# Optimization experiments

Measured on AMD Instinct MI355X. Metric: run time of the kernel, lower is better.

Reference implementation:

```python
import jax, jax.numpy as jnp
import numpy as np

B, T, V, D, H, E, K = 512, 80, 80, 128, 256, 8, 2
G1, G2 = 512, 256
EPS = 1e-5


def setup_inputs() -> dict:
    key = jax.random.key(0)
    ks = jax.random.split(key, 16)
    s = 0.05
    x = jax.random.randint(ks[0], (B, T), 0, V)
    emb = jax.random.normal(ks[1], (E, V, D), jnp.float32) * s
    Wih0 = jax.random.normal(ks[2], (E, 4 * H, D), jnp.float32) * s
    Whh0 = jax.random.normal(ks[3], (E, 4 * H, H), jnp.float32) * s
    bih0 = jnp.zeros((E, 4 * H), jnp.float32)
    bhh0 = jnp.zeros((E, 4 * H), jnp.float32)
    Wih1 = jax.random.normal(ks[4], (E, 4 * H, H), jnp.float32) * s
    Whh1 = jax.random.normal(ks[5], (E, 4 * H, H), jnp.float32) * s
    bih1 = jnp.zeros((E, 4 * H), jnp.float32)
    bhh1 = jnp.zeros((E, 4 * H), jnp.float32)
    fcw = jax.random.normal(ks[6], (E, V, H), jnp.float32) * s
    fcb = jnp.zeros((E, V), jnp.float32)
    gw1 = jax.random.normal(ks[7], (G1, D), jnp.float32) * s
    gb1 = jnp.zeros((G1,), jnp.float32)
    bn1_g = jnp.ones((G1,), jnp.float32)
    bn1_b = jnp.zeros((G1,), jnp.float32)
    bn1_m = jnp.zeros((G1,), jnp.float32)
    bn1_v = jnp.ones((G1,), jnp.float32)
    gw2 = jax.random.normal(ks[8], (G2, G1), jnp.float32) * s
    gb2 = jnp.zeros((G2,), jnp.float32)
    bn2_g = jnp.ones((G2,), jnp.float32)
    bn2_b = jnp.zeros((G2,), jnp.float32)
    bn2_m = jnp.zeros((G2,), jnp.float32)
    bn2_v = jnp.ones((G2,), jnp.float32)
    gw3 = jax.random.normal(ks[9], (E, G2), jnp.float32) * s
    gb3 = jnp.zeros((E,), jnp.float32)
    return dict(x=x, emb=emb, Wih0=Wih0, Whh0=Whh0, bih0=bih0, bhh0=bhh0,
                Wih1=Wih1, Whh1=Whh1, bih1=bih1, bhh1=bhh1, fcw=fcw, fcb=fcb,
                gw1=gw1, gb1=gb1, bn1_g=bn1_g, bn1_b=bn1_b, bn1_m=bn1_m, bn1_v=bn1_v,
                gw2=gw2, gb2=gb2, bn2_g=bn2_g, bn2_b=bn2_b, bn2_m=bn2_m, bn2_v=bn2_v,
                gw3=gw3, gb3=gb3)


def _lstm_layer(Wih, Whh, bih, bhh, xs):
    # xs: [B, T, Din] -> (hidden seq [B, T, H], final hidden [B, H]); torch gate order i,f,g,o
    h0 = jnp.zeros((xs.shape[0], Whh.shape[1]), xs.dtype)

    def step(carry, xt):
        h, c = carry
        z = xt @ Wih.T + bih + h @ Whh.T + bhh
        i, f, g, o = jnp.split(z, 4, axis=-1)
        c = jax.nn.sigmoid(f) * c + jax.nn.sigmoid(i) * jnp.tanh(g)
        h = jax.nn.sigmoid(o) * jnp.tanh(c)
        return (h, c), h

    (h, _), hs = jax.lax.scan(step, (h0, h0), jnp.swapaxes(xs, 0, 1))
    return jnp.swapaxes(hs, 0, 1), h


def _expert(emb_e, Wih0, Whh0, bih0, bhh0, Wih1, Whh1, bih1, bhh1, fcw, fcb, x):
    e = emb_e[x]                                   # [B, T, D]
    hs1, _ = _lstm_layer(Wih0, Whh0, bih0, bhh0, e)
    _, h2 = _lstm_layer(Wih1, Whh1, bih1, bhh1, hs1)
    return h2 @ fcw.T + fcb                        # [B, V] (fc on last timestep)


def _bn_eval(x, g, b, m, v):
    return (x - m) * jax.lax.rsqrt(v + EPS) * g + b


def _forward(x, emb, Wih0, Whh0, bih0, bhh0, Wih1, Whh1, bih1, bhh1, fcw, fcb,
             gw1, gb1, bn1_g, bn1_b, bn1_m, bn1_v,
             gw2, gb2, bn2_g, bn2_b, bn2_m, bn2_v, gw3, gb3):
    # gating features: expert 0 embedding, mean over time  [B, D]
    feat = emb[0][x].mean(axis=1)
    h = jax.nn.relu(_bn_eval(feat @ gw1.T + gb1, bn1_g, bn1_b, bn1_m, bn1_v))
    h = jax.nn.relu(_bn_eval(h @ gw2.T + gb2, bn2_g, bn2_b, bn2_m, bn2_v))
    logits = h @ gw3.T + gb3                       # [B, E]  (eval: no noise)
    scores = jax.nn.softmax(logits, axis=-1)
    tv, ti = jax.lax.top_k(scores, K)              # [B, K]
    w = tv / tv.sum(axis=-1, keepdims=True)
    # per-expert combine weight (top-k indices are distinct, at most one slot per expert)
    we = (w[..., None] * jax.nn.one_hot(ti, E, dtype=w.dtype)).sum(axis=1)  # [B, E]
    eouts = jax.vmap(_expert, in_axes=(0,) * 11 + (None,))(
        emb, Wih0, Whh0, bih0, bhh0, Wih1, Whh1, bih1, bhh1, fcw, fcb, x)   # [E, B, V]
    return jnp.einsum('ebc,be->bc', eouts, we)


def reference(x, emb, Wih0, Whh0, bih0, bhh0, Wih1, Whh1, bih1, bhh1, fcw, fcb,
              gw1, gb1, bn1_g, bn1_b, bn1_m, bn1_v,
              gw2, gb2, bn2_g, bn2_b, bn2_m, bn2_v, gw3, gb3):
    return _forward(x, emb, Wih0, Whh0, bih0, bhh0, Wih1, Whh1, bih1, bhh1, fcw, fcb,
                    gw1, gb1, bn1_g, bn1_b, bn1_m, bn1_v,
                    gw2, gb2, bn2_g, bn2_b, bn2_m, bn2_v, gw3, gb3)
```

## Files before the change

### kernel.cpp

```cpp
#include <hip/hip_runtime.h>
#include <hip/hip_bf16.h>
#include <math.h>

#define BB 512
#define TT 80
#define VV 80
#define DD 128
#define HH 256
#define FH 1024
#define EE 8
#define GG1 512
#define GG2 256
#define MT 16
#define NT 72
#define SLOTS (NT*MT)
#define CCK 16

typedef __attribute__((ext_vector_type(8))) short bf16x8;
typedef __attribute__((ext_vector_type(4))) float f32x4;
typedef __attribute__((ext_vector_type(4))) unsigned int u32x4;

__device__ __forceinline__ float bf2f(unsigned short u) {
    unsigned int v = ((unsigned int)u) << 16;
    return __builtin_bit_cast(float, v);
}
__device__ __forceinline__ unsigned short f2bf(float f) {
    __hip_bfloat16 h = __float2bfloat16(f);
    return __builtin_bit_cast(unsigned short, h);
}
__device__ __forceinline__ float sigm(float x) { return 1.f / (1.f + __expf(-x)); }
__device__ __forceinline__ float tanh_f(float x) {
    float ax = fabsf(x);
    float r = 1.f - 2.f / (__expf(2.f * ax) + 1.f);
    return x < 0.f ? -r : r;
}

__global__ void prep_kernel(const float* __restrict__ Whh0, const float* __restrict__ Wih1,
                            const float* __restrict__ Whh1,
                            const float* __restrict__ bih1, const float* __restrict__ bhh1,
                            unsigned short* __restrict__ WR0, unsigned short* __restrict__ WR1,
                            unsigned short* __restrict__ WG, float* __restrict__ bsum1)
{
    const int NB = 262144;
    const int ntot = 3 * NB + EE * FH;
    for (int idx = blockIdx.x * blockDim.x + threadIdx.x; idx < ntot;
         idx += gridDim.x * blockDim.x) {
        if (idx < 3 * NB) {
            int arr = idx / NB;
            int p = idx - arr * NB;
            int gc, kk, e;
            const float* src;
            if (arr < 2) {
                int l = p & 63, nf = (p >> 6) & 7, kb = (p >> 9) & 7, w = (p >> 12) & 7;
                e = (p >> 15) & 7;
                int g = nf >> 1, hc = nf & 1;
                gc = g * 256 + w * 32 + hc * 16 + (l & 15);
                kk = kb * 32 + ((l >> 4) * 8);
                src = (arr == 0) ? Whh0 : Whh1;
            } else {
                int l = p & 63, kb = (p >> 6) & 7, gf = (p >> 9) & 63; e = (p >> 15) & 7;
                gc = gf * 16 + (l & 15);
                kk = kb * 32 + ((l >> 4) * 8);
                src = Wih1;
            }
            const float* sp = src + ((size_t)e * FH + gc) * HH + kk;
            float4 f0 = *(const float4*)sp;
            float4 f1 = *(const float4*)(sp + 4);
            unsigned short out[8];
            out[0] = f2bf(f0.x); out[1] = f2bf(f0.y); out[2] = f2bf(f0.z); out[3] = f2bf(f0.w);
            out[4] = f2bf(f1.x); out[5] = f2bf(f1.y); out[6] = f2bf(f1.z); out[7] = f2bf(f1.w);
            unsigned short* dst = (arr == 0 ? WR0 : arr == 1 ? WR1 : WG) + (size_t)p * 8;
            *(uint4*)dst = *(uint4*)out;
        } else {
            int p = idx - 3 * NB;
            bsum1[p] = bih1[p] + bhh1[p];
        }
    }
}

__global__ __launch_bounds__(256)
void embw_kernel(const float* __restrict__ emb, const float* __restrict__ Wih0,
                 const float* __restrict__ bih0, const float* __restrict__ bhh0,
                 unsigned short* __restrict__ embT)
{
    const int e = blockIdx.x, g = blockIdx.y;
    const int tid = threadIdx.x;
    const int gc = g * 256 + tid;
    __shared__ float er[DD * VV];
    for (int i = tid; i < VV * DD; i += 256) {
        int tok = i >> 7, d = i & 127;
        er[d * VV + tok] = emb[((size_t)e * VV + tok) * DD + d];
    }
    __syncthreads();
    float acc[VV];
    #pragma unroll
    for (int v = 0; v < VV; v++) acc[v] = 0.f;
    const float* wr = Wih0 + ((size_t)e * FH + gc) * DD;
    for (int d = 0; d < DD; d++) {
        float wv = wr[d];
        #pragma unroll
        for (int v4 = 0; v4 < VV; v4 += 4) {
            float4 ev = *(const float4*)&er[d * VV + v4];
            acc[v4] += ev.x * wv; acc[v4 + 1] += ev.y * wv;
            acc[v4 + 2] += ev.z * wv; acc[v4 + 3] += ev.w * wv;
        }
    }
    float bias = bih0[e * FH + gc] + bhh0[e * FH + gc];
    #pragma unroll 4
    for (int v = 0; v < VV; v++)
        embT[(((size_t)e * VV + v) * 256 + tid) * 4 + g] = f2bf(acc[v] + bias);
}

__global__ __launch_bounds__(128)
void gating_kernel(const int* __restrict__ x, const float* __restrict__ emb,
                   const float* __restrict__ gw1, const float* __restrict__ gb1,
                   const float* __restrict__ g1g, const float* __restrict__ g1b,
                   const float* __restrict__ g1m, const float* __restrict__ g1v,
                   const float* __restrict__ gw2, const float* __restrict__ gb2,
                   const float* __restrict__ g2g, const float* __restrict__ g2b,
                   const float* __restrict__ g2m, const float* __restrict__ g2v,
                   const float* __restrict__ gw3, const float* __restrict__ gb3,
                   int* __restrict__ route_i, float* __restrict__ route_w)
{
    int b = blockIdx.x, tid = threadIdx.x;
    __shared__ int tk[TT];
    __shared__ float feat[DD];
    __shared__ float h1[GG1];
    __shared__ float h2[GG2];
    __shared__ float lg[EE];
    if (tid < TT) tk[tid] = x[b * TT + tid];
    __syncthreads();
    if (tid < DD) {
        float s = 0.f;
        for (int t = 0; t < TT; t++) s += emb[(size_t)tk[t] * DD + tid];
        feat[tid] = s * (1.f / TT);
    }
    __syncthreads();
    for (int j = tid; j < GG1; j += 128) {
        float s = gb1[j];
        const float* wr = gw1 + (size_t)j * DD;
        for (int d = 0; d < DD; d++) s += feat[d] * wr[d];
        float y = (s - g1m[j]) / sqrtf(g1v[j] + 1e-5f) * g1g[j] + g1b[j];
        h1[j] = y > 0.f ? y : 0.f;
    }
    __syncthreads();
    for (int j = tid; j < GG2; j += 128) {
        float s = gb2[j];
        const float* wr = gw2 + (size_t)j * GG1;
        for (int d = 0; d < GG1; d++) s += h1[d] * wr[d];
        float y = (s - g2m[j]) / sqrtf(g2v[j] + 1e-5f) * g2g[j] + g2b[j];
        h2[j] = y > 0.f ? y : 0.f;
    }
    __syncthreads();
    if (tid < EE) {
        float s = gb3[tid];
        const float* wr = gw3 + (size_t)tid * GG2;
        for (int d = 0; d < GG2; d++) s += h2[d] * wr[d];
        lg[tid] = s;
    }
    __syncthreads();
    if (tid == 0) {
        int i0 = 0;
        for (int i = 1; i < EE; i++) if (lg[i] > lg[i0]) i0 = i;
        int i1 = (i0 == 0) ? 1 : 0;
        for (int i = 0; i < EE; i++) if (i != i0 && lg[i] > lg[i1]) i1 = i;
        float e1 = expf(lg[i1] - lg[i0]);
        float inv = 1.f / (1.f + e1);
        route_i[b * 2] = i0; route_i[b * 2 + 1] = i1;
        route_w[b * 2] = inv; route_w[b * 2 + 1] = e1 * inv;
    }
}

__global__ __launch_bounds__(1024)
void route_kernel(const int* __restrict__ route_i, const float* __restrict__ route_w,
                  int* __restrict__ slot_b, int* __restrict__ slot_k,
                  float* __restrict__ slot_w, int* __restrict__ slot_e)
{
    __shared__ int wcnt[16][EE];
    __shared__ int cnt[EE];
    __shared__ int off[EE + 1];
    int tid = threadIdx.x;
    int lane = tid & 63, wv = tid >> 6;
    int e = route_i[tid];
    unsigned long long below = (1ull << lane) - 1ull;
    int rankw = 0;
    #pragma unroll
    for (int q = 0; q < EE; q++) {
        unsigned long long m = __ballot(e == q);
        if (q == e) rankw = __popcll(m & below);
        if (lane == 0) wcnt[wv][q] = __popcll(m);
    }
    __syncthreads();
    if (tid < EE) {
        int c = 0;
        for (int w2 = 0; w2 < 16; w2++) c += wcnt[w2][tid];
        cnt[tid] = c;
    }
    __syncthreads();
    if (tid == 0) {
        off[0] = 0;
        for (int q = 0; q < EE; q++) off[q + 1] = off[q] + ((cnt[q] + MT - 1) / MT) * MT;
    }
    __syncthreads();
    for (int s = tid; s < SLOTS; s += 1024) {
        int e2 = 0;
        if (s < off[EE]) { for (int q = 0; q < EE; q++) if (s >= off[q]) e2 = q; }
        slot_b[s] = -1; slot_k[s] = 0; slot_w[s] = 0.f; slot_e[s] = e2;
    }
    __syncthreads();
    int rank = rankw;
    for (int w2 = 0; w2 < wv; w2++) rank += wcnt[w2][e];
    int s = off[e] + rank;
    slot_b[s] = tid >> 1; slot_k[s] = tid & 1; slot_w[s] = route_w[tid];
}

template<int LAYER>
__device__ __forceinline__ void lstm_body(
    int t0, int tcount,
    const unsigned short* __restrict__ WR,
    const unsigned short* __restrict__ embT,
    const unsigned short* __restrict__ zin,
    const int* __restrict__ x,
    const int* __restrict__ slot_b, const int* __restrict__ slot_e,
    unsigned short* __restrict__ h0seq, float* __restrict__ h1f,
    float* __restrict__ cst, unsigned short* __restrict__ hsv,
    unsigned short (*wlds)[8][8][512], unsigned short (*hbuf)[4096], int* toks)
{
    const int tile = blockIdx.x;
    if (slot_b[tile * MT] < 0) return;
    const int tid = threadIdx.x;
    const int lane = tid & 63;
    const int w = tid >> 6;
    const int e = slot_e[tile * MT];
    const int l15 = lane & 15;
    const int q = lane >> 4;
    const int col0 = w * 32 + l15;
    const int col1 = col0 + 16;
    const int sc0 = (((col0 >> 5) * 64 + 16 * ((col0 >> 3) & 3)) << 3) + (col0 & 7);
    const int sc1 = (((col1 >> 5) * 64 + 16 * ((col1 >> 3) & 3)) << 3) + (col1 & 7);

    const unsigned short* WBg = WR + ((size_t)(e * 8 + w) * 64) * 512 + (size_t)lane * 8;

    u32x4 wres[32];
    #pragma unroll
    for (int i = 0; i < 32; i++) wres[i] = *(const u32x4*)(WBg + (size_t)i * 512);
    #pragma unroll
    for (int i = 0; i < 32; i++) asm volatile("" : "+v"(wres[i]));

    #pragma unroll
    for (int i = 0; i < 16; i++)
        *(uint4*)&wlds[i >> 3][w][i & 7][lane * 8] = *(const uint4*)(WBg + (size_t)(32 + i) * 512);

    if (LAYER == 0) {
        for (int i = tid; i < tcount * 16; i += 512)
            toks[i] = x[max(slot_b[tile * MT + (i & 15)], 0) * TT + t0 + (i >> 4)];
    }

    if (t0 == 0) {
        *(f32x4*)&hbuf[0][tid * 8] = (f32x4){0.f, 0.f, 0.f, 0.f};
    } else {
        *(bf16x8*)&hbuf[0][tid * 8] = *(const bf16x8*)(hsv + (size_t)tile * 4096 + tid * 8);
    }
    float c[8];
    if (t0 == 0) {
        #pragma unroll
        for (int i = 0; i < 8; i++) c[i] = 0.f;
    } else {
        f32x4 v0 = *(const f32x4*)&cst[((size_t)(tile * 512 + tid)) * 8];
        f32x4 v1 = *(const f32x4*)&cst[((size_t)(tile * 512 + tid)) * 8 + 4];
        c[0]=v0[0]; c[1]=v0[1]; c[2]=v0[2]; c[3]=v0[3];
        c[4]=v1[0]; c[5]=v1[1]; c[6]=v1[2]; c[7]=v1[3];
    }

    __syncthreads();

    ushort4 za[4], zb[4];
    if (LAYER == 0) {
        #pragma unroll
        for (int reg = 0; reg < 4; reg++) {
            int tok = toks[q * 4 + reg];
            const unsigned short* zp = embT + ((size_t)(e * VV + tok)) * 1024;
            za[reg] = *(const ushort4*)(zp + col0 * 4);
            zb[reg] = *(const ushort4*)(zp + col1 * 4);
        }
    } else {
        const unsigned short* zp = zin + ((size_t)(tile * tcount)) * 16384;
        #pragma unroll
        for (int g = 0; g < 4; g++) {
            int gfa = g * 16 + w * 2;
            za[g] = *(const ushort4*)(zp + (gfa * 64 + lane) * 4);
            zb[g] = *(const ushort4*)(zp + ((gfa + 1) * 64 + lane) * 4);
        }
    }

    int cur = 0;
    for (int t = 0; t < tcount; t++) {
        const int nxt = cur ^ 1;

        ushort4 zan[4], zbn[4];
        {
            int tn = (t + 1 < tcount) ? t + 1 : t;
            if (LAYER == 0) {
                #pragma unroll
                for (int reg = 0; reg < 4; reg++) {
                    int tok = toks[tn * 16 + q * 4 + reg];
                    const unsigned short* zp = embT + ((size_t)(e * VV + tok)) * 1024;
                    zan[reg] = *(const ushort4*)(zp + col0 * 4);
                    zbn[reg] = *(const ushort4*)(zp + col1 * 4);
                }
            } else {
                const unsigned short* zp = zin + ((size_t)(tile * tcount + tn)) * 16384;
                #pragma unroll
                for (int g = 0; g < 4; g++) {
                    int gfa = g * 16 + w * 2;
                    zan[g] = *(const ushort4*)(zp + (gfa * 64 + lane) * 4);
                    zbn[g] = *(const ushort4*)(zp + ((gfa + 1) * 64 + lane) * 4);
                }
            }
        }

        u32x4 ws[8];
        #pragma unroll
        for (int nf = 0; nf < 8; nf++) ws[nf] = *(const u32x4*)(WBg + (size_t)(48 + nf) * 512);

        f32x4 acc[8];
        if (LAYER == 0) {
            #pragma unroll
            for (int reg = 0; reg < 4; reg++) {
                acc[0][reg] = bf2f(za[reg].x); acc[2][reg] = bf2f(za[reg].y);
                acc[4][reg] = bf2f(za[reg].z); acc[6][reg] = bf2f(za[reg].w);
                acc[1][reg] = bf2f(zb[reg].x); acc[3][reg] = bf2f(zb[reg].y);
                acc[5][reg] = bf2f(zb[reg].z); acc[7][reg] = bf2f(zb[reg].w);
            }
        } else {
            #pragma unroll
            for (int g = 0; g < 4; g++) {
                acc[g * 2][0] = bf2f(za[g].x); acc[g * 2][1] = bf2f(za[g].y);
                acc[g * 2][2] = bf2f(za[g].z); acc[g * 2][3] = bf2f(za[g].w);
                acc[g * 2 + 1][0] = bf2f(zb[g].x); acc[g * 2 + 1][1] = bf2f(zb[g].y);
                acc[g * 2 + 1][2] = bf2f(zb[g].z); acc[g * 2 + 1][3] = bf2f(zb[g].w);
            }
        }

        #pragma unroll
        for (int kb = 0; kb < 4; kb++) {
            bf16x8 a = *(const bf16x8*)&hbuf[cur][(kb * 64 + lane) * 8];
            #pragma unroll
            for (int nf = 0; nf < 8; nf++)
                acc[nf] = __builtin_amdgcn_mfma_f32_16x16x32_bf16(
                    a, __builtin_bit_cast(bf16x8, wres[kb * 8 + nf]), acc[nf], 0, 0, 0);
        }

        #pragma unroll
        for (int kbi = 0; kbi < 2; kbi++) {
            bf16x8 a = *(const bf16x8*)&hbuf[cur][((4 + kbi) * 64 + lane) * 8];
            #pragma unroll
            for (int nf = 0; nf < 8; nf++) {
                bf16x8 wl = *(const bf16x8*)&wlds[kbi][w][nf][lane * 8];
                acc[nf] = __builtin_amdgcn_mfma_f32_16x16x32_bf16(a, wl, acc[nf], 0, 0, 0);
            }
        }

        {
            bf16x8 a = *(const bf16x8*)&hbuf[cur][(6 * 64 + lane) * 8];
            #pragma unroll
            for (int nf = 0; nf < 8; nf++)
                acc[nf] = __builtin_amdgcn_mfma_f32_16x16x32_bf16(
                    a, __builtin_bit_cast(bf16x8, ws[nf]), acc[nf], 0, 0, 0);
        }
        #pragma unroll
        for (int nf = 0; nf < 8; nf++) ws[nf] = *(const u32x4*)(WBg + (size_t)(56 + nf) * 512);
        {
            bf16x8 a = *(const bf16x8*)&hbuf[cur][(7 * 64 + lane) * 8];
            #pragma unroll
            for (int nf = 0; nf < 8; nf++)
                acc[nf] = __builtin_amdgcn_mfma_f32_16x16x32_bf16(
                    a, __builtin_bit_cast(bf16x8, ws[nf]), acc[nf], 0, 0, 0);
        }

        #pragma unroll
        for (int reg = 0; reg < 4; reg++) {
            int r = q * 4 + reg;
            {
                float iv = acc[0][reg], fv = acc[2][reg], gv = acc[4][reg], ov = acc[6][reg];
                float cn = sigm(fv) * c[reg * 2] + sigm(iv) * tanh_f(gv);
                float hn = sigm(ov) * tanh_f(cn);
                c[reg * 2] = cn;
                hbuf[nxt][sc0 + r * 8] = f2bf(hn);
                if (LAYER == 1 && t0 + t == TT - 1)
                    h1f[((size_t)(tile * MT + r)) * HH + col0] = hn;
            }
            {
                float iv = acc[1][reg], fv = acc[3][reg], gv = acc[5][reg], ov = acc[7][reg];
                float cn = sigm(fv) * c[reg * 2 + 1] + sigm(iv) * tanh_f(gv);
                float hn = sigm(ov) * tanh_f(cn);
                c[reg * 2 + 1] = cn;
                hbuf[nxt][sc1 + r * 8] = f2bf(hn);
                if (LAYER == 1 && t0 + t == TT - 1)
                    h1f[((size_t)(tile * MT + r)) * HH + col1] = hn;
            }
        }
        __syncthreads();
        cur = nxt;
        #pragma unroll
        for (int i = 0; i < 4; i++) { za[i] = zan[i]; zb[i] = zbn[i]; }
        if (LAYER == 0) {
            *(uint4*)(h0seq + ((size_t)(tile * tcount + t)) * 4096 + tid * 8) =
                *(const uint4*)&hbuf[cur][tid * 8];
        }
    }

    f32x4 v0, v1;
    v0[0]=c[0]; v0[1]=c[1]; v0[2]=c[2]; v0[3]=c[3];
    v1[0]=c[4]; v1[1]=c[5]; v1[2]=c[6]; v1[3]=c[7];
    *(f32x4*)&cst[((size_t)(tile * 512 + tid)) * 8] = v0;
    *(f32x4*)&cst[((size_t)(tile * 512 + tid)) * 8 + 4] = v1;
    *(uint4*)(hsv + (size_t)tile * 4096 + tid * 8) = *(const uint4*)&hbuf[cur][tid * 8];
}

__device__ __forceinline__ void gemm_body(
    int tcount,
    const unsigned short* __restrict__ h0seq,
    const unsigned short* __restrict__ WG,
    const float* __restrict__ bsum1,
    const int* __restrict__ slot_b, const int* __restrict__ slot_e,
    unsigned short* __restrict__ zin1,
    unsigned short* Abuf)
{
    const int tile = blockIdx.x;
    if (slot_b[tile * MT] < 0) return;
    const int tid = threadIdx.x, lane = tid & 63, w = tid >> 6;
    const int e = slot_e[tile * MT];
    const int l15 = lane & 15;
    for (int tch = 0; tch < tcount / 8; tch++) {
        const unsigned short* Asrc = h0seq + ((size_t)(tile * tcount + tch * 8)) * 4096;
        #pragma unroll
        for (int i = 0; i < 8; i++) {
            int o = (i * 512 + tid) * 8;
            *(bf16x8*)&Abuf[o] = *(const bf16x8*)&Asrc[o];
        }
        __syncthreads();
        #pragma unroll
        for (int gh = 0; gh < 2; gh++) {
            const unsigned short* Bp = WG + ((size_t)(e * 64 + w * 8 + gh * 4)) * 4096 + (size_t)lane * 8;
            f32x4 acc[8][4];
            #pragma unroll
            for (int mf = 0; mf < 8; mf++)
                #pragma unroll
                for (int nfi = 0; nfi < 4; nfi++) acc[mf][nfi] = (f32x4){0.f, 0.f, 0.f, 0.f};
            #pragma unroll
            for (int kb = 0; kb < 8; kb++) {
                bf16x8 b0 = *(const bf16x8*)(Bp + 0 * 4096 + kb * 512);
                bf16x8 b1 = *(const bf16x8*)(Bp + 1 * 4096 + kb * 512);
                bf16x8 b2 = *(const bf16x8*)(Bp + 2 * 4096 + kb * 512);
                bf16x8 b3 = *(const bf16x8*)(Bp + 3 * 4096 + kb * 512);
                #pragma unroll
                for (int mf = 0; mf < 8; mf++) {
                    bf16x8 a = *(const bf16x8*)&Abuf[(mf * 8 + kb) * 512 + lane * 8];
                    acc[mf][0] = __builtin_amdgcn_mfma_f32_16x16x32_bf16(a, b0, acc[mf][0], 0, 0, 0);
                    acc[mf][1] = __builtin_amdgcn_mfma_f32_16x16x32_bf16(a, b1, acc[mf][1], 0, 0, 0);
                    acc[mf][2] = __builtin_amdgcn_mfma_f32_16x16x32_bf16(a, b2, acc[mf][2], 0, 0, 0);
                    acc[mf][3] = __builtin_amdgcn_mfma_f32_16x16x32_bf16(a, b3, acc[mf][3], 0, 0, 0);
                }
            }
            #pragma unroll
            for (int mf = 0; mf < 8; mf++) {
                unsigned short* ob = zin1 + ((size_t)(tile * tcount + tch * 8 + mf)) * 16384;
                #pragma unroll
                for (int nfi = 0; nfi < 4; nfi++) {
                    int gf = w * 8 + gh * 4 + nfi;
                    float bs = bsum1[e * FH + gf * 16 + l15];
                    ushort4 v;
                    v.x = f2bf(acc[mf][nfi][0] + bs);
                    v.y = f2bf(acc[mf][nfi][1] + bs);
                    v.z = f2bf(acc[mf][nfi][2] + bs);
                    v.w = f2bf(acc[mf][nfi][3] + bs);
                    *(ushort4*)(ob + (size_t)(gf * 64 + lane) * 4) = v;
                }
            }
        }
        __syncthreads();
    }
}

__global__ __launch_bounds__(512, 1)
void lstm_fused(int t00, int t01, int tg, int tcount,
                const unsigned short* __restrict__ WR0, const unsigned short* __restrict__ WR1,
                const unsigned short* __restrict__ WG, const float* __restrict__ bsum1,
                const unsigned short* __restrict__ embT,
                unsigned short* __restrict__ h0_w, const unsigned short* __restrict__ h0_r,
                unsigned short* __restrict__ zin_w, const unsigned short* __restrict__ zin_r,
                const int* __restrict__ x,
                const int* __restrict__ slot_b, const int* __restrict__ slot_e,
                float* __restrict__ h1f,
                float* __restrict__ cst0, float* __restrict__ cst1,
                unsigned short* __restrict__ hsv0, unsigned short* __restrict__ hsv1)
{
    __shared__ unsigned short wlds[2][8][8][512];
    __shared__ unsigned short hbuf[2][4096];
    __shared__ int toks[CCK * 16];
    if (blockIdx.y == 0) {
        if (t00 < 0) return;
        lstm_body<0>(t00, tcount, WR0, embT, nullptr, x, slot_b, slot_e,
                     h0_w, h1f, cst0, hsv0, wlds, hbuf, toks);
    } else if (blockIdx.y == 1) {
        if (t01 < 0) return;
        lstm_body<1>(t01, tcount, WR1, embT, zin_r, x, slot_b, slot_e,
                     nullptr, h1f, cst1, hsv1, wlds, hbuf, toks);
    } else {
        if (tg < 0) return;
        gemm_body(tcount, h0_r, WG, bsum1, slot_b, slot_e, zin_w, &wlds[0][0][0][0]);
    }
}

__global__ __launch_bounds__(256)
void fc_kernel(const float* __restrict__ fcw, const float* __restrict__ fcb,
               const float* __restrict__ h1f,
               const int* __restrict__ slot_b, const int* __restrict__ slot_k,
               const float* __restrict__ slot_w, const int* __restrict__ slot_e,
               float* __restrict__ wout)
{
    int s = blockIdx.x;
    int b = slot_b[s];
    if (b < 0) return;
    int tid = threadIdx.x;
    __shared__ float hv[HH];
    if (tid < HH) hv[tid] = h1f[(size_t)s * HH + tid];
    __syncthreads();
    int e = slot_e[s], kk = slot_k[s];
    float w = slot_w[s];
    for (int v = tid; v < VV; v += 256) {
        float sacc = fcb[e * VV + v];
        const float* fr = fcw + ((size_t)e * VV + v) * HH;
        #pragma unroll 4
        for (int d = 0; d < HH; d++) sacc += hv[d] * fr[d];
        wout[((size_t)b * 2 + kk) * VV + v] = w * sacc;
    }
}

__global__ void combine_kernel(const float* __restrict__ wout, float* __restrict__ out)
{
    int i = blockIdx.x * blockDim.x + threadIdx.x;
    if (i < BB * VV) {
        int b = i / VV, v = i % VV;
        out[i] = wout[((size_t)b * 2) * VV + v] + wout[((size_t)b * 2 + 1) * VV + v];
    }
}

extern "C" void kernel_launch(void* const* d_in, const int* in_sizes, int n_in,
                              void* d_out, int out_size, void* d_ws, size_t ws_size,
                              hipStream_t stream)
{
    const int*   x    = (const int*)d_in[0];
    const float* emb  = (const float*)d_in[1];
    const float* Wih0 = (const float*)d_in[2];
    const float* Whh0 = (const float*)d_in[3];
    const float* bih0 = (const float*)d_in[4];
    const float* bhh0 = (const float*)d_in[5];
    const float* Wih1 = (const float*)d_in[6];
    const float* Whh1 = (const float*)d_in[7];
    const float* bih1 = (const float*)d_in[8];
    const float* bhh1 = (const float*)d_in[9];
    const float* fcw  = (const float*)d_in[10];
    const float* fcb  = (const float*)d_in[11];
    const float* gw1  = (const float*)d_in[12];
    const float* gb1  = (const float*)d_in[13];
    const float* b1g  = (const float*)d_in[14];
    const float* b1b  = (const float*)d_in[15];
    const float* b1m  = (const float*)d_in[16];
    const float* b1v  = (const float*)d_in[17];
    const float* gw2  = (const float*)d_in[18];
    const float* gb2  = (const float*)d_in[19];
    const float* b2g  = (const float*)d_in[20];
    const float* b2b  = (const float*)d_in[21];
    const float* b2m  = (const float*)d_in[22];
    const float* b2v  = (const float*)d_in[23];
    const float* gw3  = (const float*)d_in[24];
    const float* gb3  = (const float*)d_in[25];

    const size_t NWsh = 262144 * 8;

    char* base = (char*)d_ws;
    size_t o = 0;
    auto alloc = [&](size_t bytes) { char* p = base + o; o = (o + bytes + 255) & ~(size_t)255; return p; };

    unsigned short* WR0  = (unsigned short*)alloc(NWsh * 2);
    unsigned short* WR1  = (unsigned short*)alloc(NWsh * 2);
    unsigned short* WG   = (unsigned short*)alloc(NWsh * 2);
    unsigned short* embT = (unsigned short*)alloc((size_t)EE * VV * FH * 2);
    float* bsum1 = (float*)alloc((size_t)EE * FH * 4);
    float* h1f   = (float*)alloc((size_t)SLOTS * HH * 4);
    float* wout  = (float*)alloc((size_t)BB * 2 * VV * 4);
    float* cst0  = (float*)alloc((size_t)NT * 512 * 8 * 4);
    float* cst1  = (float*)alloc((size_t)NT * 512 * 8 * 4);
    unsigned short* hsv0 = (unsigned short*)alloc((size_t)NT * 4096 * 2);
    unsigned short* hsv1 = (unsigned short*)alloc((size_t)NT * 4096 * 2);
    float* route_w = (float*)alloc((size_t)BB * 2 * 4);
    float* slot_w  = (float*)alloc((size_t)SLOTS * 4);
    int* route_i = (int*)alloc((size_t)BB * 2 * 4);
    int* slot_b  = (int*)alloc((size_t)SLOTS * 4);
    int* slot_k  = (int*)alloc((size_t)SLOTS * 4);
    int* slot_e  = (int*)alloc((size_t)SLOTS * 4);
    unsigned short* h0seqA = (unsigned short*)alloc((size_t)NT * CCK * 4096 * 2);
    unsigned short* h0seqB = (unsigned short*)alloc((size_t)NT * CCK * 4096 * 2);
    unsigned short* zinA   = (unsigned short*)alloc((size_t)NT * CCK * 16384 * 2);
    unsigned short* zinB   = (unsigned short*)alloc((size_t)NT * CCK * 16384 * 2);

    prep_kernel<<<3104, 256, 0, stream>>>(Whh0, Wih1, Whh1, bih1, bhh1, WR0, WR1, WG, bsum1);
    embw_kernel<<<dim3(EE, 4), 256, 0, stream>>>(emb, Wih0, bih0, bhh0, embT);
    gating_kernel<<<BB, 128, 0, stream>>>(x, emb, gw1, gb1, b1g, b1b, b1m, b1v,
                                          gw2, gb2, b2g, b2b, b2m, b2v, gw3, gb3,
                                          route_i, route_w);
    route_kernel<<<1, 1024, 0, stream>>>(route_i, route_w, slot_b, slot_k, slot_w, slot_e);

    const int nch = TT / CCK;
    for (int ph = 0; ph <= nch + 1; ph++) {
        int t00 = (ph < nch) ? ph * CCK : -1;
        int tg  = (ph - 1 >= 0 && ph - 1 < nch) ? (ph - 1) * CCK : -1;
        int t01 = (ph - 2 >= 0 && ph - 2 < nch) ? (ph - 2) * CCK : -1;
        unsigned short* h0_w = (ph & 1) ? h0seqB : h0seqA;
        unsigned short* h0_r = ((ph - 1) & 1) ? h0seqB : h0seqA;
        unsigned short* zn_w = ((ph - 1) & 1) ? zinB : zinA;
        unsigned short* zn_r = ((ph - 2) & 1) ? zinB : zinA;
        lstm_fused<<<dim3(NT, 3), 512, 0, stream>>>(t00, t01, tg, CCK, WR0, WR1, WG, bsum1,
                                                    embT, h0_w, h0_r, zn_w, zn_r, x,
                                                    slot_b, slot_e, h1f,
                                                    cst0, cst1, hsv0, hsv1);
    }

    fc_kernel<<<SLOTS, 256, 0, stream>>>(fcw, fcb, h1f, slot_b, slot_k, slot_w, slot_e, wout);
    combine_kernel<<<(BB * VV + 255) / 256, 256, 0, stream>>>(wout, (float*)d_out);
}
```

Before: 775.4 us.

## Replace per-phase kernel launches with one persistent cooperative kernel using grid sync

```diff
diff --git a/kernel.cpp b/kernel.cpp
--- a/kernel.cpp
+++ b/kernel.cpp
@@ -1,6 +1,9 @@
 #include <hip/hip_runtime.h>
 #include <hip/hip_bf16.h>
+#include <hip/hip_cooperative_groups.h>
 #include <math.h>
+
+namespace cg = cooperative_groups;
 
 #define BB 512
 #define TT 80
@@ -15,6 +18,8 @@
 #define NT 72
 #define SLOTS (NT*MT)
 #define CCK 16
+#define NCH (TT/CCK)
+#define NPH (NCH+2)
 
 typedef __attribute__((ext_vector_type(8))) short bf16x8;
 typedef __attribute__((ext_vector_type(4))) float f32x4;
@@ -215,23 +220,16 @@
 }
 
 template<int LAYER>
-__device__ __forceinline__ void lstm_body(
-    int t0, int tcount,
-    const unsigned short* __restrict__ WR,
+__device__ __forceinline__ void lstm_chunk(
+    int t0, int tile, int e, int lane, int w,
+    const unsigned short* __restrict__ WBg,
     const unsigned short* __restrict__ embT,
     const unsigned short* __restrict__ zin,
-    const int* __restrict__ x,
-    const int* __restrict__ slot_b, const int* __restrict__ slot_e,
-    unsigned short* __restrict__ h0seq, float* __restrict__ h1f,
-    float* __restrict__ cst, unsigned short* __restrict__ hsv,
-    unsigned short (*wlds)[8][8][512], unsigned short (*hbuf)[4096], int* toks)
-{
-    const int tile = blockIdx.x;
-    if (slot_b[tile * MT] < 0) return;
-    const int tid = threadIdx.x;
-    const int lane = tid & 63;
-    const int w = tid >> 6;
-    const int e = slot_e[tile * MT];
+    unsigned short* __restrict__ h0_w, float* __restrict__ h1f,
+    u32x4 (&wres)[32],
+    unsigned short (*wlds)[8][8][512], unsigned short (*hbuf)[4096], int* toks,
+    float (&c)[8], int& cur)
+{
     const int l15 = lane & 15;
     const int q = lane >> 4;
     const int col0 = w * 32 + l15;
@@ -239,52 +237,17 @@
     const int sc0 = (((col0 >> 5) * 64 + 16 * ((col0 >> 3) & 3)) << 3) + (col0 & 7);
     const int sc1 = (((col1 >> 5) * 64 + 16 * ((col1 >> 3) & 3)) << 3) + (col1 & 7);
 
-    const unsigned short* WBg = WR + ((size_t)(e * 8 + w) * 64) * 512 + (size_t)lane * 8;
-
-    u32x4 wres[32];
-    #pragma unroll
-    for (int i = 0; i < 32; i++) wres[i] = *(const u32x4*)(WBg + (size_t)i * 512);
-    #pragma unroll
-    for (int i = 0; i < 32; i++) asm volatile("" : "+v"(wres[i]));
-
-    #pragma unroll
-    for (int i = 0; i < 16; i++)
-        *(uint4*)&wlds[i >> 3][w][i & 7][lane * 8] = *(const uint4*)(WBg + (size_t)(32 + i) * 512);
-
-    if (LAYER == 0) {
-        for (int i = tid; i < tcount * 16; i += 512)
-            toks[i] = x[max(slot_b[tile * MT + (i & 15)], 0) * TT + t0 + (i >> 4)];
-    }
-
-    if (t0 == 0) {
-        *(f32x4*)&hbuf[0][tid * 8] = (f32x4){0.f, 0.f, 0.f, 0.f};
-    } else {
-        *(bf16x8*)&hbuf[0][tid * 8] = *(const bf16x8*)(hsv + (size_t)tile * 4096 + tid * 8);
-    }
-    float c[8];
-    if (t0 == 0) {
-        #pragma unroll
-        for (int i = 0; i < 8; i++) c[i] = 0.f;
-    } else {
-        f32x4 v0 = *(const f32x4*)&cst[((size_t)(tile * 512 + tid)) * 8];
-        f32x4 v1 = *(const f32x4*)&cst[((size_t)(tile * 512 + tid)) * 8 + 4];
-        c[0]=v0[0]; c[1]=v0[1]; c[2]=v0[2]; c[3]=v0[3];
-        c[4]=v1[0]; c[5]=v1[1]; c[6]=v1[2]; c[7]=v1[3];
-    }
-
-    __syncthreads();
-
     ushort4 za[4], zb[4];
     if (LAYER == 0) {
         #pragma unroll
         for (int reg = 0; reg < 4; reg++) {
-            int tok = toks[q * 4 + reg];
+            int tok = toks[t0 * 16 + q * 4 + reg];
             const unsigned short* zp = embT + ((size_t)(e * VV + tok)) * 1024;
             za[reg] = *(const ushort4*)(zp + col0 * 4);
             zb[reg] = *(const ushort4*)(zp + col1 * 4);
         }
     } else {
-        const unsigned short* zp = zin + ((size_t)(tile * tcount)) * 16384;
+        const unsigned short* zp = zin + ((size_t)(tile * CCK)) * 16384;
         #pragma unroll
         for (int g = 0; g < 4; g++) {
             int gfa = g * 16 + w * 2;
@@ -293,23 +256,22 @@
         }
     }
 
-    int cur = 0;
-    for (int t = 0; t < tcount; t++) {
+    for (int t = 0; t < CCK; t++) {
         const int nxt = cur ^ 1;
 
         ushort4 zan[4], zbn[4];
         {
-            int tn = (t + 1 < tcount) ? t + 1 : t;
+            int tn = (t + 1 < CCK) ? t + 1 : t;
             if (LAYER == 0) {
                 #pragma unroll
                 for (int reg = 0; reg < 4; reg++) {
-                    int tok = toks[tn * 16 + q * 4 + reg];
+                    int tok = toks[(t0 + tn) * 16 + q * 4 + reg];
                     const unsigned short* zp = embT + ((size_t)(e * VV + tok)) * 1024;
                     zan[reg] = *(const ushort4*)(zp + col0 * 4);
                     zbn[reg] = *(const ushort4*)(zp + col1 * 4);
                 }
             } else {
-                const unsigned short* zp = zin + ((size_t)(tile * tcount + tn)) * 16384;
+                const unsigned short* zp = zin + ((size_t)(tile * CCK + tn)) * 16384;
                 #pragma unroll
                 for (int g = 0; g < 4; g++) {
                     int gfa = g * 16 + w * 2;
@@ -350,7 +312,6 @@
                 acc[nf] = __builtin_amdgcn_mfma_f32_16x16x32_bf16(
                     a, __builtin_bit_cast(bf16x8, wres[kb * 8 + nf]), acc[nf], 0, 0, 0);
         }
-
         #pragma unroll
         for (int kbi = 0; kbi < 2; kbi++) {
             bf16x8 a = *(const bf16x8*)&hbuf[cur][((4 + kbi) * 64 + lane) * 8];
@@ -360,7 +321,6 @@
                 acc[nf] = __builtin_amdgcn_mfma_f32_16x16x32_bf16(a, wl, acc[nf], 0, 0, 0);
             }
         }
-
         {
             bf16x8 a = *(const bf16x8*)&hbuf[cur][(6 * 64 + lane) * 8];
             #pragma unroll
@@ -405,35 +365,24 @@
         #pragma unroll
         for (int i = 0; i < 4; i++) { za[i] = zan[i]; zb[i] = zbn[i]; }
         if (LAYER == 0) {
-            *(uint4*)(h0seq + ((size_t)(tile * tcount + t)) * 4096 + tid * 8) =
-                *(const uint4*)&hbuf[cur][tid * 8];
-        }
-    }
-
-    f32x4 v0, v1;
-    v0[0]=c[0]; v0[1]=c[1]; v0[2]=c[2]; v0[3]=c[3];
-    v1[0]=c[4]; v1[1]=c[5]; v1[2]=c[6]; v1[3]=c[7];
-    *(f32x4*)&cst[((size_t)(tile * 512 + tid)) * 8] = v0;
-    *(f32x4*)&cst[((size_t)(tile * 512 + tid)) * 8 + 4] = v1;
-    *(uint4*)(hsv + (size_t)tile * 4096 + tid * 8) = *(const uint4*)&hbuf[cur][tid * 8];
-}
-
-__device__ __forceinline__ void gemm_body(
-    int tcount,
-    const unsigned short* __restrict__ h0seq,
+            *(uint4*)(h0_w + ((size_t)(tile * CCK + t)) * 4096 + threadIdx.x * 8) =
+                *(const uint4*)&hbuf[cur][threadIdx.x * 8];
+        }
+    }
+}
+
+__device__ __forceinline__ void gemm_chunk(
+    int tile, int e, int lane, int w,
+    const unsigned short* __restrict__ h0_r,
     const unsigned short* __restrict__ WG,
     const float* __restrict__ bsum1,
-    const int* __restrict__ slot_b, const int* __restrict__ slot_e,
-    unsigned short* __restrict__ zin1,
+    unsigned short* __restrict__ zin_w,
     unsigned short* Abuf)
 {
-    const int tile = blockIdx.x;
-    if (slot_b[tile * MT] < 0) return;
-    const int tid = threadIdx.x, lane = tid & 63, w = tid >> 6;
-    const int e = slot_e[tile * MT];
+    const int tid = threadIdx.x;
     const int l15 = lane & 15;
-    for (int tch = 0; tch < tcount / 8; tch++) {
-        const unsigned short* Asrc = h0seq + ((size_t)(tile * tcount + tch * 8)) * 4096;
+    for (int tch = 0; tch < CCK / 8; tch++) {
+        const unsigned short* Asrc = h0_r + ((size_t)(tile * CCK + tch * 8)) * 4096;
         #pragma unroll
         for (int i = 0; i < 8; i++) {
             int o = (i * 512 + tid) * 8;
@@ -465,7 +414,7 @@
             }
             #pragma unroll
             for (int mf = 0; mf < 8; mf++) {
-                unsigned short* ob = zin1 + ((size_t)(tile * tcount + tch * 8 + mf)) * 16384;
+                unsigned short* ob = zin_w + ((size_t)(tile * CCK + tch * 8 + mf)) * 16384;
                 #pragma unroll
                 for (int nfi = 0; nfi < 4; nfi++) {
                     int gf = w * 8 + gh * 4 + nfi;
@@ -484,32 +433,73 @@
 }
 
 __global__ __launch_bounds__(512, 1)
-void lstm_fused(int t00, int t01, int tg, int tcount,
-                const unsigned short* __restrict__ WR0, const unsigned short* __restrict__ WR1,
-                const unsigned short* __restrict__ WG, const float* __restrict__ bsum1,
-                const unsigned short* __restrict__ embT,
-                unsigned short* __restrict__ h0_w, const unsigned short* __restrict__ h0_r,
-                unsigned short* __restrict__ zin_w, const unsigned short* __restrict__ zin_r,
-                const int* __restrict__ x,
-                const int* __restrict__ slot_b, const int* __restrict__ slot_e,
-                float* __restrict__ h1f,
-                float* __restrict__ cst0, float* __restrict__ cst1,
-                unsigned short* __restrict__ hsv0, unsigned short* __restrict__ hsv1)
-{
+void pipeline_kernel(const unsigned short* __restrict__ WR0,
+                     const unsigned short* __restrict__ WR1,
+                     const unsigned short* __restrict__ WG,
+                     const float* __restrict__ bsum1,
+                     const unsigned short* __restrict__ embT,
+                     unsigned short* __restrict__ h0A, unsigned short* __restrict__ h0B,
+                     unsigned short* __restrict__ zinA, unsigned short* __restrict__ zinB,
+                     const int* __restrict__ x,
+                     const int* __restrict__ slot_b, const int* __restrict__ slot_e,
+                     float* __restrict__ h1f)
+{
+    cg::grid_group grid = cg::this_grid();
+    const int tile = blockIdx.x;
+    const int slice = blockIdx.y;
+    const int tid = threadIdx.x;
+    const int lane = tid & 63;
+    const int w = tid >> 6;
+    const bool valid = (slot_b[tile * MT] >= 0);
+    const int e = slot_e[tile * MT];
+
     __shared__ unsigned short wlds[2][8][8][512];
     __shared__ unsigned short hbuf[2][4096];
-    __shared__ int toks[CCK * 16];
-    if (blockIdx.y == 0) {
-        if (t00 < 0) return;
-        lstm_body<0>(t00, tcount, WR0, embT, nullptr, x, slot_b, slot_e,
-                     h0_w, h1f, cst0, hsv0, wlds, hbuf, toks);
-    } else if (blockIdx.y == 1) {
-        if (t01 < 0) return;
-        lstm_body<1>(t01, tcount, WR1, embT, zin_r, x, slot_b, slot_e,
-                     nullptr, h1f, cst1, hsv1, wlds, hbuf, toks);
-    } else {
-        if (tg < 0) return;
-        gemm_body(tcount, h0_r, WG, bsum1, slot_b, slot_e, zin_w, &wlds[0][0][0][0]);
+    __shared__ int toks[TT * 16];
+
+    u32x4 wres[32];
+    const unsigned short* WBg = nullptr;
+    if (slice < 2 && valid) {
+        WBg = (slice ? WR1 : WR0) + ((size_t)(e * 8 + w) * 64) * 512 + (size_t)lane * 8;
+        #pragma unroll
+        for (int i = 0; i < 32; i++) wres[i] = *(const u32x4*)(WBg + (size_t)i * 512);
+        #pragma unroll
+        for (int i = 0; i < 32; i++) asm volatile("" : "+v"(wres[i]));
+        #pragma unroll
+        for (int i = 0; i < 16; i++)
+            *(uint4*)&wlds[i >> 3][w][i & 7][lane * 8] = *(const uint4*)(WBg + (size_t)(32 + i) * 512);
+        if (slice == 0) {
+            for (int i = tid; i < TT * 16; i += 512)
+                toks[i] = x[max(slot_b[tile * MT + (i & 15)], 0) * TT + (i >> 4)];
+        }
+        *(f32x4*)&hbuf[0][tid * 8] = (f32x4){0.f, 0.f, 0.f, 0.f};
+    }
+    float c[8];
+    #pragma unroll
+    for (int i = 0; i < 8; i++) c[i] = 0.f;
+    int cur = 0;
+    if (slice < 2 && valid) __syncthreads();
+
+    for (int ph = 0; ph < NPH; ph++) {
+        if (valid) {
+            if (slice == 0 && ph < NCH) {
+                unsigned short* h0_w = (ph & 1) ? h0B : h0A;
+                lstm_chunk<0>(ph * CCK, tile, e, lane, w, WBg, embT, nullptr,
+                              h0_w, h1f, wres, wlds, hbuf, toks, c, cur);
+            } else if (slice == 2 && ph >= 1 && ph <= NCH) {
+                int ch = ph - 1;
+                const unsigned short* h0_r = (ch & 1) ? h0B : h0A;
+                unsigned short* zn_w = (ch & 1) ? zinB : zinA;
+                gemm_chunk(tile, e, lane, w, h0_r, WG, bsum1, zn_w, &wlds[0][0][0][0]);
+            } else if (slice == 1 && ph >= 2) {
+                int ch = ph - 2;
+                const unsigned short* zn_r = (ch & 1) ? zinB : zinA;
+                lstm_chunk<1>(ch * CCK, tile, e, lane, w, WBg, embT, zn_r,
+                              nullptr, h1f, wres, wlds, hbuf, toks, c, cur);
+            }
+        }
+        __threadfence();
+        grid.sync();
     }
 }
 
@@ -591,20 +581,16 @@
     float* bsum1 = (float*)alloc((size_t)EE * FH * 4);
     float* h1f   = (float*)alloc((size_t)SLOTS * HH * 4);
     float* wout  = (float*)alloc((size_t)BB * 2 * VV * 4);
-    float* cst0  = (float*)alloc((size_t)NT * 512 * 8 * 4);
-    float* cst1  = (float*)alloc((size_t)NT * 512 * 8 * 4);
-    unsigned short* hsv0 = (unsigned short*)alloc((size_t)NT * 4096 * 2);
-    unsigned short* hsv1 = (unsigned short*)alloc((size_t)NT * 4096 * 2);
     float* route_w = (float*)alloc((size_t)BB * 2 * 4);
     float* slot_w  = (float*)alloc((size_t)SLOTS * 4);
     int* route_i = (int*)alloc((size_t)BB * 2 * 4);
     int* slot_b  = (int*)alloc((size_t)SLOTS * 4);
     int* slot_k  = (int*)alloc((size_t)SLOTS * 4);
     int* slot_e  = (int*)alloc((size_t)SLOTS * 4);
-    unsigned short* h0seqA = (unsigned short*)alloc((size_t)NT * CCK * 4096 * 2);
-    unsigned short* h0seqB = (unsigned short*)alloc((size_t)NT * CCK * 4096 * 2);
-    unsigned short* zinA   = (unsigned short*)alloc((size_t)NT * CCK * 16384 * 2);
-    unsigned short* zinB   = (unsigned short*)alloc((size_t)NT * CCK * 16384 * 2);
+    unsigned short* h0A  = (unsigned short*)alloc((size_t)NT * CCK * 4096 * 2);
+    unsigned short* h0B  = (unsigned short*)alloc((size_t)NT * CCK * 4096 * 2);
+    unsigned short* zinA = (unsigned short*)alloc((size_t)NT * CCK * 16384 * 2);
+    unsigned short* zinB = (unsigned short*)alloc((size_t)NT * CCK * 16384 * 2);
 
     prep_kernel<<<3104, 256, 0, stream>>>(Whh0, Wih1, Whh1, bih1, bhh1, WR0, WR1, WG, bsum1);
     embw_kernel<<<dim3(EE, 4), 256, 0, stream>>>(emb, Wih0, bih0, bhh0, embT);
@@ -613,19 +599,12 @@
                                           route_i, route_w);
     route_kernel<<<1, 1024, 0, stream>>>(route_i, route_w, slot_b, slot_k, slot_w, slot_e);
 
-    const int nch = TT / CCK;
-    for (int ph = 0; ph <= nch + 1; ph++) {
-        int t00 = (ph < nch) ? ph * CCK : -1;
-        int tg  = (ph - 1 >= 0 && ph - 1 < nch) ? (ph - 1) * CCK : -1;
-        int t01 = (ph - 2 >= 0 && ph - 2 < nch) ? (ph - 2) * CCK : -1;
-        unsigned short* h0_w = (ph & 1) ? h0seqB : h0seqA;
-        unsigned short* h0_r = ((ph - 1) & 1) ? h0seqB : h0seqA;
-        unsigned short* zn_w = ((ph - 1) & 1) ? zinB : zinA;
-        unsigned short* zn_r = ((ph - 2) & 1) ? zinB : zinA;
-        lstm_fused<<<dim3(NT, 3), 512, 0, stream>>>(t00, t01, tg, CCK, WR0, WR1, WG, bsum1,
-                                                    embT, h0_w, h0_r, zn_w, zn_r, x,
-                                                    slot_b, slot_e, h1f,
-                                                    cst0, cst1, hsv0, hsv1);
+    {
+        void* args[] = { (void*)&WR0, (void*)&WR1, (void*)&WG, (void*)&bsum1, (void*)&embT,
+                         (void*)&h0A, (void*)&h0B, (void*)&zinA, (void*)&zinB,
+                         (void*)&x, (void*)&slot_b, (void*)&slot_e, (void*)&h1f };
+        hipLaunchCooperativeKernel((const void*)pipeline_kernel, dim3(NT, 3), dim3(512),
+                                   args, 0, stream);
     }
 
     fc_kernel<<<SLOTS, 256, 0, stream>>>(fcw, fcb, h1f, slot_b, slot_k, slot_w, slot_e, wout);
```

After: 1.334 ms. 1.72x slower.
